# Optimization experiments

Hardware: AMD Instinct MI355X
Metric: run time of the kernel (lower is better)

Reference implementation:

```python
import jax, jax.numpy as jnp
import numpy as np

N, E, D_IN, D_OUT = 50000, 800000, 128, 128
LN_EPS = 1e-5


def setup_inputs() -> dict:
    key = jax.random.key(0)
    ks = jax.random.split(key, 7)
    x = jax.random.normal(ks[0], (N, D_IN), dtype=jnp.float32)
    adj = jax.random.randint(ks[1], (2, E), 0, N, dtype=jnp.int32)  # edge_index
    scale = 1.0 / np.sqrt(D_IN)
    W_gcn = jax.random.normal(ks[2], (D_IN, D_OUT), dtype=jnp.float32) * scale
    b_gcn = jax.random.normal(ks[3], (D_OUT,), dtype=jnp.float32) * 0.02
    W_lin = jax.random.normal(ks[4], (D_IN, D_OUT), dtype=jnp.float32) * scale
    ln_w = jnp.ones((D_OUT,), dtype=jnp.float32)
    ln_b = jnp.zeros((D_OUT,), dtype=jnp.float32)
    return {"adj": adj, "x": x, "W_gcn": W_gcn, "b_gcn": b_gcn,
            "W_lin": W_lin, "ln_w": ln_w, "ln_b": ln_b}


def _gcn_conv(x, edge_index, W, b):
    """PyG GCNConv: add self-loops, symmetric D^-1/2 (A+I) D^-1/2 normalization."""
    n = x.shape[0]
    loop = jnp.arange(n, dtype=edge_index.dtype)
    src = jnp.concatenate([edge_index[0], loop])  # message sources (x_j)
    dst = jnp.concatenate([edge_index[1], loop])  # aggregation targets
    ones = jnp.ones(src.shape[0], dtype=x.dtype)
    deg = jax.ops.segment_sum(ones, dst, num_segments=n)
    dinv = jnp.where(deg > 0, jax.lax.rsqrt(deg), 0.0)
    norm = dinv[src] * dinv[dst]                   # [E+N]
    h = x @ W                                      # [N, D_OUT] project first (PyG order)
    msg = h[src] * norm[:, None]                   # gather + scale
    agg = jax.ops.segment_sum(msg, dst, num_segments=n)
    return agg + b


def _layer_norm(y, w, b):
    mu = jnp.mean(y, axis=-1, keepdims=True)
    var = jnp.mean(jnp.square(y - mu), axis=-1, keepdims=True)
    return (y - mu) * jax.lax.rsqrt(var + LN_EPS) * w + b


def reference(adj, x, W_gcn, b_gcn, W_lin, ln_w, ln_b):
    x1 = _gcn_conv(x, adj, W_gcn, b_gcn)
    x2 = x @ W_lin                                  # bias=False linear
    return _layer_norm(x1 + x2 + 1e-6, ln_w, ln_b)
```

## Files before the change

kernel.cpp:

```cpp
#include <hip/hip_runtime.h>
#include <hip/hip_bf16.h>

#define NN 50000
#define EE 800000
#define DD 128
#define CB 196
#define NFB 1563
#define EBLK 2048
#define NEBK 391
#define XSB 3125
#define SSZ 5120

typedef __attribute__((ext_vector_type(8))) short bf16x8;
typedef __attribute__((ext_vector_type(4))) float f32x4;

static __device__ __forceinline__ unsigned short f2bf(float f) {
  union { float f; unsigned u; } v; v.f = f;
  unsigned r = v.u + 0x7FFFu + ((v.u >> 16) & 1u);
  return (unsigned short)(r >> 16);
}
static __device__ __forceinline__ float bf2f(unsigned short h) {
  union { unsigned u; float f; } v; v.u = ((unsigned)h) << 16;
  return v.f;
}

__global__ __launch_bounds__(256) void k_p0(
    const int* __restrict__ dst, int* __restrict__ hist,
    const float* __restrict__ Wg, const float* __restrict__ Wl,
    unsigned short* __restrict__ Wt, const float4* __restrict__ x4,
    ushort4* __restrict__ xb4) {
  int b = blockIdx.x, t = threadIdx.x;
  if (b < NEBK) {
    __shared__ int cnt[CB];
    for (int i = t; i < CB; i += 256) cnt[i] = 0;
    __syncthreads();
    int e0 = b * EBLK;
    for (int i = t; i < EBLK; i += 256) {
      int e = e0 + i;
      if (e < EE) atomicAdd(&cnt[dst[e] >> 8], 1);
    }
    __syncthreads();
    for (int i = t; i < CB; i += 256) hist[b * CB + i] = cnt[i];
  } else if (b < NEBK + 32) {
    for (int i = (b - NEBK) * 256 + t; i < DD * 256; i += 32 * 256) {
      int n = i >> 8, k = i & 255;
      float v = (k < 128) ? Wg[k * DD + n] : Wl[(k - 128) * DD + n];
      Wt[i] = f2bf(v);
    }
  } else {
    int base = (b - NEBK - 32) * 1024 + t;
#pragma unroll
    for (int k = 0; k < 4; k++) {
      int i = base + k * 256;
      if (i < NN * 32) {
        float4 v = x4[i];
        ushort4 o;
        o.x = f2bf(v.x); o.y = f2bf(v.y); o.z = f2bf(v.z); o.w = f2bf(v.w);
        xb4[i] = o;
      }
    }
  }
}

__global__ __launch_bounds__(512) void k_scatter(
    const int* __restrict__ src, const int* __restrict__ dst,
    const int* __restrict__ hist, int* __restrict__ coarseTot,
    unsigned int* __restrict__ pairs) {
  __shared__ unsigned int rec[EBLK];
  __shared__ unsigned int sorted[EBLK];
  __shared__ int tot[CB], chunk[CB], own[CB], cur[CB], gofs[CB];
  __shared__ int sc[256];
  int blk = blockIdx.x, t = threadIdx.x;
  int e0 = blk * EBLK;
  int vcnt = EE - e0; if (vcnt > EBLK) vcnt = EBLK;
  for (int i = t; i < vcnt; i += 512) {
    int d = dst[e0 + i], s = src[e0 + i];
    rec[i] = (unsigned int)s | ((unsigned int)(d & 255) << 16) |
             ((unsigned int)(d >> 8) << 24);
  }
  if (t < CB) {
    int to = 0, ch = 0, ow = 0;
    for (int b2 = 0; b2 < NEBK; ++b2) {
      int v = hist[b2 * CB + t];
      to += v;
      ch += (b2 < blk) ? v : 0;
      ow = (b2 == blk) ? v : ow;
    }
    tot[t] = to; chunk[t] = ch; own[t] = ow;
    if (blk == 0) coarseTot[t] = to;
  }
  __syncthreads();
  if (t < 256) sc[t] = (t < CB) ? tot[t] : 0;
  for (int off = 1; off < 256; off <<= 1) {
    __syncthreads();
    int tmp = (t < 256 && t >= off) ? sc[t - off] : 0;
    __syncthreads();
    if (t < 256 && t >= off) sc[t] += tmp;
  }
  __syncthreads();
  if (t < CB) gofs[t] = (sc[t] - tot[t]) + chunk[t];
  __syncthreads();
  if (t < 256) sc[t] = (t < CB) ? own[t] : 0;
  for (int off = 1; off < 256; off <<= 1) {
    __syncthreads();
    int tmp = (t < 256 && t >= off) ? sc[t - off] : 0;
    __syncthreads();
    if (t < 256 && t >= off) sc[t] += tmp;
  }
  __syncthreads();
  if (t < CB) {
    int lo = sc[t] - own[t];
    cur[t] = lo;
    gofs[t] -= lo;
  }
  __syncthreads();
  for (int i = t; i < vcnt; i += 512) {
    unsigned int r = rec[i];
    int cb = r >> 24;
    int p = atomicAdd(&cur[cb], 1);
    sorted[p] = r;
  }
  __syncthreads();
  for (int i = t; i < vcnt; i += 512) {
    unsigned int r = sorted[i];
    pairs[gofs[r >> 24] + i] = r;
  }
}

__global__ __launch_bounds__(512) void k_p1b(
    const unsigned int* __restrict__ pairs, const int* __restrict__ coarseTot,
    int* __restrict__ deg, float* __restrict__ dinv, int* __restrict__ rowStart,
    unsigned short* __restrict__ srcU16) {
  __shared__ int ldeg[256], lscan[256], lcur[256];
  __shared__ int wsum[8];
  __shared__ unsigned short ssrc[SSZ];
  int b = blockIdx.x, t = threadIdx.x;
  int n0 = b << 8;
  int nloc = NN - n0; if (nloc > 256) nloc = 256;
  int partial = 0;
  for (int i = t; i < b; i += 512) partial += coarseTot[i];
#pragma unroll
  for (int off = 32; off > 0; off >>= 1) partial += __shfl_xor(partial, off);
  if ((t & 63) == 0) wsum[t >> 6] = partial;
  if (t < 256) ldeg[t] = 0;
  __syncthreads();
  int start = wsum[0] + wsum[1] + wsum[2] + wsum[3] +
              wsum[4] + wsum[5] + wsum[6] + wsum[7];
  int cnt = coarseTot[b];
  for (int i = t; i < cnt; i += 512)
    atomicAdd(&ldeg[(pairs[start + i] >> 16) & 255], 1);
  __syncthreads();
  int dg = (t < 256) ? ldeg[t] : 0;
  if (t < 256) lscan[t] = dg;
  for (int off = 1; off < 256; off <<= 1) {
    __syncthreads();
    int tmp = (t < 256 && t >= off) ? lscan[t - off] : 0;
    __syncthreads();
    if (t < 256 && t >= off) lscan[t] += tmp;
  }
  __syncthreads();
  bool useStage = (cnt <= SSZ);
  if (t < 256) {
    int lofs = lscan[t] - dg;
    lcur[t] = lofs;
    if (t < nloc) {
      deg[n0 + t] = dg;
      dinv[n0 + t] = rsqrtf((float)(dg + 1));
      rowStart[n0 + t] = start + lofs;
    }
  }
  __syncthreads();
  for (int i = t; i < cnt; i += 512) {
    unsigned int pr = pairs[start + i];
    int pos = atomicAdd(&lcur[(pr >> 16) & 255], 1);
    unsigned short v = (unsigned short)(pr & 0xFFFFu);
    if (useStage) ssrc[pos] = v;
    else          srcU16[start + pos] = v;
  }
  if (useStage) {
    __syncthreads();
    for (int i = t; i < cnt; i += 512) srcU16[start + i] = ssrc[i];
  }
}

__global__ __launch_bounds__(256) void k_xs(
    const unsigned short* __restrict__ xb, const float* __restrict__ dinv,
    unsigned short* __restrict__ xs) {
  int i = blockIdx.x * 256 + threadIdx.x;
  int row = i >> 4;
  float di = dinv[row];
  bf16x8 v = *(const bf16x8*)(xb + (size_t)i * 8);
  bf16x8 o;
#pragma unroll
  for (int k = 0; k < 8; k++) o[k] = (short)f2bf(bf2f((unsigned short)v[k]) * di);
  *(bf16x8*)(xs + (size_t)i * 8) = o;
}

static __device__ __forceinline__ void gather16(
    const unsigned short* __restrict__ xs, const unsigned short* __restrict__ srcU16,
    int js, int cnt, int r, int srcLaneBase, float* acc) {
  for (int base = 0; base < cnt; base += 16) {
    int idx = (base + r < cnt) ? (int)srcU16[js + base + r] : 0;
    int m = cnt - base; if (m > 16) m = 16;
    int j = 0;
    for (; j + 8 <= m; j += 8) {
      int s0 = __shfl(idx, srcLaneBase + j);
      int s1 = __shfl(idx, srcLaneBase + j + 1);
      int s2 = __shfl(idx, srcLaneBase + j + 2);
      int s3 = __shfl(idx, srcLaneBase + j + 3);
      int s4 = __shfl(idx, srcLaneBase + j + 4);
      int s5 = __shfl(idx, srcLaneBase + j + 5);
      int s6 = __shfl(idx, srcLaneBase + j + 6);
      int s7 = __shfl(idx, srcLaneBase + j + 7);
      bf16x8 v0 = *(const bf16x8*)(xs + (size_t)s0 * DD + r * 8);
      bf16x8 v1 = *(const bf16x8*)(xs + (size_t)s1 * DD + r * 8);
      bf16x8 v2 = *(const bf16x8*)(xs + (size_t)s2 * DD + r * 8);
      bf16x8 v3 = *(const bf16x8*)(xs + (size_t)s3 * DD + r * 8);
      bf16x8 v4 = *(const bf16x8*)(xs + (size_t)s4 * DD + r * 8);
      bf16x8 v5 = *(const bf16x8*)(xs + (size_t)s5 * DD + r * 8);
      bf16x8 v6 = *(const bf16x8*)(xs + (size_t)s6 * DD + r * 8);
      bf16x8 v7 = *(const bf16x8*)(xs + (size_t)s7 * DD + r * 8);
#pragma unroll
      for (int k = 0; k < 8; k++) acc[k] += bf2f((unsigned short)v0[k]);
#pragma unroll
      for (int k = 0; k < 8; k++) acc[k] += bf2f((unsigned short)v1[k]);
#pragma unroll
      for (int k = 0; k < 8; k++) acc[k] += bf2f((unsigned short)v2[k]);
#pragma unroll
      for (int k = 0; k < 8; k++) acc[k] += bf2f((unsigned short)v3[k]);
#pragma unroll
      for (int k = 0; k < 8; k++) acc[k] += bf2f((unsigned short)v4[k]);
#pragma unroll
      for (int k = 0; k < 8; k++) acc[k] += bf2f((unsigned short)v5[k]);
#pragma unroll
      for (int k = 0; k < 8; k++) acc[k] += bf2f((unsigned short)v6[k]);
#pragma unroll
      for (int k = 0; k < 8; k++) acc[k] += bf2f((unsigned short)v7[k]);
    }
    for (; j < m; j++) {
      int s = __shfl(idx, srcLaneBase + j);
      bf16x8 v = *(const bf16x8*)(xs + (size_t)s * DD + r * 8);
#pragma unroll
      for (int k = 0; k < 8; k++) acc[k] += bf2f((unsigned short)v[k]);
    }
  }
}

__global__ __launch_bounds__(512) void k_mega4(
    const unsigned short* __restrict__ xs, const unsigned short* __restrict__ xb,
    const int* __restrict__ rowStart, const int* __restrict__ deg,
    const unsigned short* __restrict__ srcU16, const float* __restrict__ dinv,
    const unsigned short* __restrict__ Wt, const float* __restrict__ bgcn,
    const float* __restrict__ lnw, const float* __restrict__ lnb,
    float* __restrict__ out) {
  __shared__ unsigned short abuf[32 * 136];
  int b = blockIdx.x, t = threadIdx.x;
  int n0 = b * 32;
  int g = t >> 4, r = t & 15;
  int lane = t & 63;
  int srcLaneBase = lane & 48;
  int node = n0 + g;
  bool valid = (node < NN);
  int nc = valid ? node : (NN - 1);
  float acc[8];
  {
    bf16x8 va = *(const bf16x8*)(xs + (size_t)nc * DD + r * 8);
#pragma unroll
    for (int k = 0; k < 8; k++) acc[k] = bf2f((unsigned short)va[k]);
  }
  int js = valid ? rowStart[nc] : 0;
  int cnt = valid ? deg[nc] : 0;
  gather16(xs, srcU16, js, cnt, r, srcLaneBase, acc);
  {
    float d = dinv[nc];
    bf16x8 o;
#pragma unroll
    for (int k = 0; k < 8; k++) o[k] = valid ? (short)f2bf(acc[k] * d) : (short)0;
    *(bf16x8*)&abuf[g * 136 + r * 8] = o;
  }
  __syncthreads();
  if (t < 128) {
    int w = t >> 6, lane2 = t & 63;
    int quad = lane2 >> 4, rr = lane2 & 15;
    int mloc = w * 16 + rr;
    int rowA = n0 + mloc; int rc = (rowA < NN) ? rowA : (NN - 1);
    f32x4 zero = {0.f, 0.f, 0.f, 0.f};
    f32x4 macc[8];
#pragma unroll
    for (int i = 0; i < 8; i++) macc[i] = zero;
#pragma unroll
    for (int ks = 0; ks < 8; ks++) {
      bf16x8 a;
      if (ks < 4) a = *(const bf16x8*)&abuf[mloc * 136 + ks * 32 + quad * 8];
      else        a = *(const bf16x8*)(xb + (size_t)rc * DD + (ks - 4) * 32 + quad * 8);
#pragma unroll
      for (int nt = 0; nt < 8; nt++) {
        bf16x8 bb = *(const bf16x8*)(Wt + (size_t)(nt * 16 + rr) * 256 + ks * 32 + quad * 8);
        macc[nt] = __builtin_amdgcn_mfma_f32_16x16x32_bf16(a, bb, macc[nt], 0, 0, 0);
      }
    }
    float bg[8], lw[8], lb[8];
#pragma unroll
    for (int nt = 0; nt < 8; nt++) {
      int col = nt * 16 + rr;
      bg[nt] = bgcn[col] + 1e-6f;
      lw[nt] = lnw[col];
      lb[nt] = lnb[col];
    }
#pragma unroll
    for (int reg = 0; reg < 4; reg++) {
      float y[8];
      float s1 = 0.f, s2 = 0.f;
#pragma unroll
      for (int nt = 0; nt < 8; nt++) {
        y[nt] = macc[nt][reg] + bg[nt];
        s1 += y[nt];
        s2 += y[nt] * y[nt];
      }
#pragma unroll
      for (int off = 1; off < 16; off <<= 1) {
        s1 += __shfl_xor(s1, off);
        s2 += __shfl_xor(s2, off);
      }
      float mu = s1 * (1.0f / 128.0f);
      float var = s2 * (1.0f / 128.0f) - mu * mu;
      float inv = rsqrtf(var + 1e-5f);
      int row = n0 + w * 16 + quad * 4 + reg;
      if (row < NN) {
#pragma unroll
        for (int nt = 0; nt < 8; nt++) {
          out[(size_t)row * DD + nt * 16 + rr] = (y[nt] - mu) * inv * lw[nt] + lb[nt];
        }
      }
    }
  }
}

extern "C" void kernel_launch(void* const* d_in, const int* in_sizes, int n_in,
                              void* d_out, int out_size, void* d_ws, size_t ws_size,
                              hipStream_t stream) {
  const int* adj = (const int*)d_in[0];
  const float* x = (const float*)d_in[1];
  const float* Wg = (const float*)d_in[2];
  const float* bg = (const float*)d_in[3];
  const float* Wl = (const float*)d_in[4];
  const float* lw = (const float*)d_in[5];
  const float* lb = (const float*)d_in[6];
  const int* srcp = adj;
  const int* dstp = adj + EE;
  float* out = (float*)d_out;

  char* ws = (char*)d_ws;
  size_t off = 0;
  auto alloc = [&](size_t bytes) -> void* {
    void* p = ws + off;
    off += (bytes + 255) & ~(size_t)255;
    return p;
  };
  int* hist = (int*)alloc((size_t)NEBK * CB * 4);
  int* coarseTot = (int*)alloc((size_t)256 * 4);
  unsigned int* pairs = (unsigned int*)alloc((size_t)EE * 4);
  unsigned short* srcU16 = (unsigned short*)alloc((size_t)EE * 2);
  int* deg = (int*)alloc((size_t)NN * 4);
  float* dinv = (float*)alloc((size_t)NN * 4);
  int* rowStart = (int*)alloc((size_t)NN * 4);
  unsigned short* xb = (unsigned short*)alloc((size_t)NN * DD * 2);
  unsigned short* xs = (unsigned short*)alloc((size_t)NN * DD * 2);
  unsigned short* Wt = (unsigned short*)alloc((size_t)DD * 256 * 2);
  (void)ws_size; (void)in_sizes; (void)n_in; (void)out_size;

  k_p0<<<NEBK + 32 + 1563, 256, 0, stream>>>(dstp, hist, Wg, Wl, Wt,
                                             (const float4*)x, (ushort4*)xb);
  k_scatter<<<NEBK, 512, 0, stream>>>(srcp, dstp, hist, coarseTot, pairs);
  k_p1b<<<CB, 512, 0, stream>>>(pairs, coarseTot, deg, dinv, rowStart, srcU16);
  k_xs<<<XSB, 256, 0, stream>>>(xb, dinv, xs);
  k_mega4<<<NFB, 512, 0, stream>>>(xs, xb, rowStart, deg, srcU16, dinv, Wt,
                                   bg, lw, lb, out);
}
```

Before: 200.1 us.

## Transpose histogram, merge scans, fuse xs scaling into CSR build kernel

The histogram is stored transposed and padded so that each k_scatter thread reads its bucket row with vectorized uint4 loads, split across two half-blocks. The two prefix scans are packed into a single scan of a combined (total<<12 | own) value, and block 0 writes bucket base and total arrays so k_p1b no longer rescans coarse totals. k_p1b also writes srcU16 directly without LDS staging and now does the dinv scaling of xb into xs, which removes a separate kernel launch. The packed scan assumes per-block bucket counts stay below 4096, and the fused xs work runs on only 196 blocks.

```diff
diff --git a/kernel.cpp b/kernel.cpp
--- a/kernel.cpp
+++ b/kernel.cpp
@@ -8,8 +8,7 @@
 #define NFB 1563
 #define EBLK 2048
 #define NEBK 391
-#define XSB 3125
-#define SSZ 5120
+#define HST 392
 
 typedef __attribute__((ext_vector_type(8))) short bf16x8;
 typedef __attribute__((ext_vector_type(4))) float f32x4;
@@ -40,7 +39,10 @@
       if (e < EE) atomicAdd(&cnt[dst[e] >> 8], 1);
     }
     __syncthreads();
-    for (int i = t; i < CB; i += 256) hist[b * CB + i] = cnt[i];
+    if (t < CB) {
+      hist[t * HST + b] = cnt[t];
+      if (b == 0) hist[t * HST + (HST - 1)] = 0;
+    }
   } else if (b < NEBK + 32) {
     for (int i = (b - NEBK) * 256 + t; i < DD * 256; i += 32 * 256) {
       int n = i >> 8, k = i & 255;
@@ -64,12 +66,13 @@
 
 __global__ __launch_bounds__(512) void k_scatter(
     const int* __restrict__ src, const int* __restrict__ dst,
-    const int* __restrict__ hist, int* __restrict__ coarseTot,
-    unsigned int* __restrict__ pairs) {
+    const int* __restrict__ hist, int* __restrict__ bucketBase,
+    int* __restrict__ bucketTot, unsigned int* __restrict__ pairs) {
   __shared__ unsigned int rec[EBLK];
   __shared__ unsigned int sorted[EBLK];
-  __shared__ int tot[CB], chunk[CB], own[CB], cur[CB], gofs[CB];
-  __shared__ int sc[256];
+  __shared__ int sTo[2][CB], sCh[2][CB], sOw[2][CB];
+  __shared__ unsigned int sc[256];
+  __shared__ int cur[CB], gofs[CB];
   int blk = blockIdx.x, t = threadIdx.x;
   int e0 = blk * EBLK;
   int vcnt = EE - e0; if (vcnt > EBLK) vcnt = EBLK;
@@ -78,46 +81,52 @@
     rec[i] = (unsigned int)s | ((unsigned int)(d & 255) << 16) |
              ((unsigned int)(d >> 8) << 24);
   }
+  int q = t & 255, h = t >> 8;
+  if (q < CB) {
+    const uint4* hp = (const uint4*)(hist + (size_t)q * HST + h * (HST / 2));
+    int cb0 = h * (HST / 2);
+    int to = 0, ch = 0, ow = 0;
+#pragma unroll 7
+    for (int v = 0; v < HST / 8; ++v) {
+      uint4 hv = hp[v];
+      int c = cb0 + v * 4;
+      int a0 = (int)hv.x, a1 = (int)hv.y, a2 = (int)hv.z, a3 = (int)hv.w;
+      to += a0 + a1 + a2 + a3;
+      ch += (c + 0 < blk ? a0 : 0) + (c + 1 < blk ? a1 : 0) +
+            (c + 2 < blk ? a2 : 0) + (c + 3 < blk ? a3 : 0);
+      ow += (c + 0 == blk ? a0 : 0) + (c + 1 == blk ? a1 : 0) +
+            (c + 2 == blk ? a2 : 0) + (c + 3 == blk ? a3 : 0);
+    }
+    sTo[h][q] = to; sCh[h][q] = ch; sOw[h][q] = ow;
+  }
+  __syncthreads();
+  int totv = 0, chpv = 0, ownv = 0;
   if (t < CB) {
-    int to = 0, ch = 0, ow = 0;
-    for (int b2 = 0; b2 < NEBK; ++b2) {
-      int v = hist[b2 * CB + t];
-      to += v;
-      ch += (b2 < blk) ? v : 0;
-      ow = (b2 == blk) ? v : ow;
-    }
-    tot[t] = to; chunk[t] = ch; own[t] = ow;
-    if (blk == 0) coarseTot[t] = to;
-  }
-  __syncthreads();
-  if (t < 256) sc[t] = (t < CB) ? tot[t] : 0;
+    totv = sTo[0][t] + sTo[1][t];
+    chpv = sCh[0][t] + sCh[1][t];
+    ownv = sOw[0][t] + sOw[1][t];
+  }
+  if (t < 256) sc[t] = (t < CB) ? (((unsigned)totv << 12) | (unsigned)ownv) : 0u;
   for (int off = 1; off < 256; off <<= 1) {
     __syncthreads();
-    int tmp = (t < 256 && t >= off) ? sc[t - off] : 0;
+    unsigned tmp = (t < 256 && t >= off) ? sc[t - off] : 0u;
     __syncthreads();
     if (t < 256 && t >= off) sc[t] += tmp;
   }
   __syncthreads();
-  if (t < CB) gofs[t] = (sc[t] - tot[t]) + chunk[t];
-  __syncthreads();
-  if (t < 256) sc[t] = (t < CB) ? own[t] : 0;
-  for (int off = 1; off < 256; off <<= 1) {
-    __syncthreads();
-    int tmp = (t < 256 && t >= off) ? sc[t - off] : 0;
-    __syncthreads();
-    if (t < 256 && t >= off) sc[t] += tmp;
-  }
-  __syncthreads();
   if (t < CB) {
-    int lo = sc[t] - own[t];
+    unsigned v = sc[t];
+    int incT = (int)(v >> 12), incO = (int)(v & 4095u);
+    int gb = incT - totv;
+    int lo = incO - ownv;
     cur[t] = lo;
-    gofs[t] -= lo;
+    gofs[t] = gb + chpv - lo;
+    if (blk == 0) { bucketBase[t] = gb; bucketTot[t] = totv; }
   }
   __syncthreads();
   for (int i = t; i < vcnt; i += 512) {
     unsigned int r = rec[i];
-    int cb = r >> 24;
-    int p = atomicAdd(&cur[cb], 1);
+    int p = atomicAdd(&cur[r >> 24], 1);
     sorted[p] = r;
   }
   __syncthreads();
@@ -128,25 +137,19 @@
 }
 
 __global__ __launch_bounds__(512) void k_p1b(
-    const unsigned int* __restrict__ pairs, const int* __restrict__ coarseTot,
+    const unsigned int* __restrict__ pairs, const int* __restrict__ bucketBase,
+    const int* __restrict__ bucketTot, const unsigned short* __restrict__ xb,
     int* __restrict__ deg, float* __restrict__ dinv, int* __restrict__ rowStart,
-    unsigned short* __restrict__ srcU16) {
+    unsigned short* __restrict__ srcU16, unsigned short* __restrict__ xs) {
   __shared__ int ldeg[256], lscan[256], lcur[256];
-  __shared__ int wsum[8];
-  __shared__ unsigned short ssrc[SSZ];
+  __shared__ float ldinvs[256];
   int b = blockIdx.x, t = threadIdx.x;
   int n0 = b << 8;
   int nloc = NN - n0; if (nloc > 256) nloc = 256;
-  int partial = 0;
-  for (int i = t; i < b; i += 512) partial += coarseTot[i];
-#pragma unroll
-  for (int off = 32; off > 0; off >>= 1) partial += __shfl_xor(partial, off);
-  if ((t & 63) == 0) wsum[t >> 6] = partial;
+  int start = bucketBase[b];
+  int cnt = bucketTot[b];
   if (t < 256) ldeg[t] = 0;
   __syncthreads();
-  int start = wsum[0] + wsum[1] + wsum[2] + wsum[3] +
-              wsum[4] + wsum[5] + wsum[6] + wsum[7];
-  int cnt = coarseTot[b];
   for (int i = t; i < cnt; i += 512)
     atomicAdd(&ldeg[(pairs[start + i] >> 16) & 255], 1);
   __syncthreads();
@@ -159,41 +162,28 @@
     if (t < 256 && t >= off) lscan[t] += tmp;
   }
   __syncthreads();
-  bool useStage = (cnt <= SSZ);
   if (t < 256) {
-    int lofs = lscan[t] - dg;
-    lcur[t] = lofs;
-    if (t < nloc) {
-      deg[n0 + t] = dg;
-      dinv[n0 + t] = rsqrtf((float)(dg + 1));
-      rowStart[n0 + t] = start + lofs;
-    }
+    int rs = start + lscan[t] - dg;
+    lcur[t] = rs;
+    float di = rsqrtf((float)(dg + 1));
+    ldinvs[t] = di;
+    if (t < nloc) { deg[n0 + t] = dg; dinv[n0 + t] = di; rowStart[n0 + t] = rs; }
   }
   __syncthreads();
   for (int i = t; i < cnt; i += 512) {
     unsigned int pr = pairs[start + i];
     int pos = atomicAdd(&lcur[(pr >> 16) & 255], 1);
-    unsigned short v = (unsigned short)(pr & 0xFFFFu);
-    if (useStage) ssrc[pos] = v;
-    else          srcU16[start + pos] = v;
-  }
-  if (useStage) {
-    __syncthreads();
-    for (int i = t; i < cnt; i += 512) srcU16[start + i] = ssrc[i];
-  }
-}
-
-__global__ __launch_bounds__(256) void k_xs(
-    const unsigned short* __restrict__ xb, const float* __restrict__ dinv,
-    unsigned short* __restrict__ xs) {
-  int i = blockIdx.x * 256 + threadIdx.x;
-  int row = i >> 4;
-  float di = dinv[row];
-  bf16x8 v = *(const bf16x8*)(xb + (size_t)i * 8);
-  bf16x8 o;
-#pragma unroll
-  for (int k = 0; k < 8; k++) o[k] = (short)f2bf(bf2f((unsigned short)v[k]) * di);
-  *(bf16x8*)(xs + (size_t)i * 8) = o;
+    srcU16[pos] = (unsigned short)(pr & 0xFFFFu);
+  }
+  for (int i = t; i < nloc * 16; i += 512) {
+    int rr = i >> 4, qq = i & 15;
+    bf16x8 v = *(const bf16x8*)(xb + (size_t)(n0 + rr) * DD + qq * 8);
+    float di = ldinvs[rr];
+    bf16x8 o;
+#pragma unroll
+    for (int k = 0; k < 8; k++) o[k] = (short)f2bf(bf2f((unsigned short)v[k]) * di);
+    *(bf16x8*)(xs + (size_t)(n0 + rr) * DD + qq * 8) = o;
+  }
 }
 
 static __device__ __forceinline__ void gather16(
@@ -357,8 +347,9 @@
     off += (bytes + 255) & ~(size_t)255;
     return p;
   };
-  int* hist = (int*)alloc((size_t)NEBK * CB * 4);
-  int* coarseTot = (int*)alloc((size_t)256 * 4);
+  int* hist = (int*)alloc((size_t)CB * HST * 4);
+  int* bucketBase = (int*)alloc((size_t)256 * 4);
+  int* bucketTot = (int*)alloc((size_t)256 * 4);
   unsigned int* pairs = (unsigned int*)alloc((size_t)EE * 4);
   unsigned short* srcU16 = (unsigned short*)alloc((size_t)EE * 2);
   int* deg = (int*)alloc((size_t)NN * 4);
@@ -371,9 +362,10 @@
 
   k_p0<<<NEBK + 32 + 1563, 256, 0, stream>>>(dstp, hist, Wg, Wl, Wt,
                                              (const float4*)x, (ushort4*)xb);
-  k_scatter<<<NEBK, 512, 0, stream>>>(srcp, dstp, hist, coarseTot, pairs);
-  k_p1b<<<CB, 512, 0, stream>>>(pairs, coarseTot, deg, dinv, rowStart, srcU16);
-  k_xs<<<XSB, 256, 0, stream>>>(xb, dinv, xs);
+  k_scatter<<<NEBK, 512, 0, stream>>>(srcp, dstp, hist, bucketBase, bucketTot,
+                                      pairs);
+  k_p1b<<<CB, 512, 0, stream>>>(pairs, bucketBase, bucketTot, xb, deg, dinv,
+                                rowStart, srcU16, xs);
   k_mega4<<<NFB, 512, 0, stream>>>(xs, xb, rowStart, deg, srcU16, dinv, Wt,
                                    bg, lw, lb, out);
 }
```

New measurement: 187.1 us. 1.07x faster.
